# Kernel tuning notes

Measured on AMD Instinct MI355X. Metric: run time of the kernel, lower is better.

## Reference

```python
import jax, jax.numpy as jnp
import numpy as np

B, S, D, H = 2, 2048, 512, 8
HD = D // H
DFF = 4 * D
EPS_LN = 1e-5
EPS_ATTN = 1e-8


def layernorm(x, w, b):
    mu = jnp.mean(x, axis=-1, keepdims=True)
    var = jnp.var(x, axis=-1, keepdims=True)
    return (x - mu) * jax.lax.rsqrt(var + EPS_LN) * w + b


def masked_attention(q_src, v_src, wq, bq, wk, bk, wv, bv, wo, bo, M):
    # q_src/v_src: (B,S,D); M: (B,S,S)
    Bs, Ss, _ = q_src.shape
    Q = (q_src @ wq + bq).reshape(Bs, Ss, H, HD)
    K = (q_src @ wk + bk).reshape(Bs, Ss, H, HD)
    V = (v_src @ wv + bv).reshape(Bs, Ss, H, HD)
    scale = HD ** -0.5
    scores = jnp.einsum('bqhd,bkhd->bhqk', Q, K) * scale
    Mh = M[:, None, :, :]                      # (B,1,S,S) broadcast over heads
    scores = scores * Mh
    A = jax.nn.softmax(scores, axis=-1)
    A = A * Mh                                 # re-mask post-softmax
    A = A / (jnp.sum(jnp.abs(A), axis=-1, keepdims=True) + EPS_ATTN)  # L1 renorm
    out = jnp.einsum('bhqk,bkhd->bqhd', A, V).reshape(Bs, Ss, D)
    return out @ wo + bo


def ffn(x, w1, b1, w2, b2):
    h = jax.nn.gelu(x @ w1 + b1, approximate=False)
    return x + (h @ w2 + b2)                   # FeedForward(num_layers=2) includes residual


def setup_inputs() -> dict:
    key = jax.random.key(0)
    ks = iter(jax.random.split(key, 64))
    nrm = lambda shape, s=0.02: jax.random.normal(next(ks), shape, jnp.float32) * s
    d = {
        'gene_emb': jax.random.normal(next(ks), (B, S, D), jnp.float32),
        'expr_emb': jax.random.normal(next(ks), (B, S, D), jnp.float32),
        'M': jax.random.uniform(next(ks), (B, S, S), jnp.float32),
    }
    # gene attention params (weights stored (in,out))
    for p in ['g_wq', 'g_wk', 'g_wv', 'g_wo']:
        d[p] = nrm((D, D))
    for p in ['g_bq', 'g_bk', 'g_bv', 'g_bo']:
        d[p] = jnp.zeros((D,), jnp.float32)
    # expr attention params (fused proj 2D->D)
    d['e_wf'] = nrm((2 * D, D)); d['e_bf'] = jnp.zeros((D,), jnp.float32)
    for p in ['e_wq', 'e_wk', 'e_wv', 'e_wo']:
        d[p] = nrm((D, D))
    for p in ['e_bq', 'e_bk', 'e_bv', 'e_bo']:
        d[p] = jnp.zeros((D,), jnp.float32)
    # layernorms
    for p in ['ln_g1_w', 'ln_g2_w', 'ln_e1_w', 'ln_e2_w']:
        d[p] = jnp.ones((D,), jnp.float32)
    for p in ['ln_g1_b', 'ln_g2_b', 'ln_e1_b', 'ln_e2_b']:
        d[p] = jnp.zeros((D,), jnp.float32)
    # FFNs
    d['fg_w1'] = nrm((D, DFF)); d['fg_b1'] = jnp.zeros((DFF,), jnp.float32)
    d['fg_w2'] = nrm((DFF, D)); d['fg_b2'] = jnp.zeros((D,), jnp.float32)
    d['fe_w1'] = nrm((D, DFF)); d['fe_b1'] = jnp.zeros((DFF,), jnp.float32)
    d['fe_w2'] = nrm((DFF, D)); d['fe_b2'] = jnp.zeros((D,), jnp.float32)
    return d


def reference(gene_emb, expr_emb, M,
              g_wq, g_bq, g_wk, g_bk, g_wv, g_bv, g_wo, g_bo,
              e_wf, e_bf, e_wq, e_bq, e_wk, e_bk, e_wv, e_bv, e_wo, e_bo,
              ln_g1_w, ln_g1_b, ln_g2_w, ln_g2_b,
              ln_e1_w, ln_e1_b, ln_e2_w, ln_e2_b,
              fg_w1, fg_b1, fg_w2, fg_b2,
              fe_w1, fe_b1, fe_w2, fe_b2):
    # ----- gene branch -----
    xg = layernorm(gene_emb, ln_g1_w, ln_g1_b)
    attn_g = masked_attention(xg, xg, g_wq, g_bq, g_wk, g_bk, g_wv, g_bv, g_wo, g_bo, M)
    x = gene_emb + attn_g
    x_ln = layernorm(x, ln_g2_w, ln_g2_b)
    out_gene = x + ffn(x_ln, fg_w1, fg_b1, fg_w2, fg_b2)
    # ----- expression branch -----
    y_n = layernorm(expr_emb, ln_e1_w, ln_e1_b)
    fused = jnp.concatenate([gene_emb, y_n], axis=-1) @ e_wf + e_bf
    attn_e = masked_attention(fused, y_n, e_wq, e_bq, e_wk, e_bk, e_wv, e_bv, e_wo, e_bo, M)
    y = expr_emb + attn_e
    y_ln = layernorm(y, ln_e2_w, ln_e2_b)
    out_expr = y + ffn(y_ln, fe_w1, fe_b1, fe_w2, fe_b2)
    return (out_gene, out_expr)
```

## Files before the change

### kernel.cpp

```cpp
#include <hip/hip_runtime.h>
#include <math.h>

#define S_LEN 2048
#define DMODEL 512
#define NROWS 4096
#define NHEAD 8
#define HDIM 64
#define LOG2E 1.4426950408889634f

typedef __attribute__((ext_vector_type(8))) __bf16 bf16x8;
typedef __attribute__((ext_vector_type(4))) float f32x4;

__device__ inline float bf2f(unsigned short h) {
    unsigned u = ((unsigned)h) << 16;
    return __builtin_bit_cast(float, u);
}
__device__ inline unsigned short f2bf(float f) {
    unsigned u = __builtin_bit_cast(unsigned, f);
    return (unsigned short)((u + 0x7fffu + ((u >> 16) & 1u)) >> 16);
}

__device__ inline void gl_lds16(const unsigned short* g, unsigned short* l) {
    __builtin_amdgcn_global_load_lds(
        (const __attribute__((address_space(1))) void*)g,
        (__attribute__((address_space(3))) void*)l, 16, 0, 0);
}

__global__ __launch_bounds__(256) void wcast_t(
    const float* __restrict__ W, unsigned short* __restrict__ Wt, int K, int Mo)
{
    __shared__ float t[32][33];
    const int bx = blockIdx.x * 32;
    const int by = blockIdx.y * 32;
    const int tx = threadIdx.x & 31, ty = threadIdx.x >> 5;
    #pragma unroll
    for (int r = 0; r < 4; ++r)
        t[ty + 8 * r][tx] = W[(size_t)(by + ty + 8 * r) * Mo + bx + tx];
    __syncthreads();
    #pragma unroll
    for (int r = 0; r < 4; ++r)
        Wt[(size_t)(bx + ty + 8 * r) * K + by + tx] = f2bf(t[tx][ty + 8 * r]);
}

__global__ __launch_bounds__(256) void wcast_sq8(
    const float* w0, const float* w1, const float* w2, const float* w3,
    const float* w4, const float* w5, const float* w6, const float* w7,
    unsigned short* __restrict__ dst)
{
    const float* srcs[8] = {w0, w1, w2, w3, w4, w5, w6, w7};
    const float* __restrict__ W = srcs[blockIdx.z];
    unsigned short* __restrict__ Wt = dst + (size_t)blockIdx.z * 512 * 512;
    __shared__ float t[32][33];
    const int bx = blockIdx.x * 32, by = blockIdx.y * 32;
    const int tx = threadIdx.x & 31, ty = threadIdx.x >> 5;
    #pragma unroll
    for (int r = 0; r < 4; ++r)
        t[ty + 8 * r][tx] = W[(size_t)(by + ty + 8 * r) * 512 + bx + tx];
    __syncthreads();
    #pragma unroll
    for (int r = 0; r < 4; ++r)
        Wt[(size_t)(bx + ty + 8 * r) * 512 + by + tx] = f2bf(t[tx][ty + 8 * r]);
}

__global__ __launch_bounds__(256) void wcast_t2(
    const float* wA, const float* wB, unsigned short* __restrict__ dst,
    int K, int Mo)
{
    const float* __restrict__ W = blockIdx.z ? wB : wA;
    unsigned short* __restrict__ Wt = dst + (size_t)blockIdx.z * K * Mo;
    __shared__ float t[32][33];
    const int bx = blockIdx.x * 32, by = blockIdx.y * 32;
    const int tx = threadIdx.x & 31, ty = threadIdx.x >> 5;
    #pragma unroll
    for (int r = 0; r < 4; ++r)
        t[ty + 8 * r][tx] = W[(size_t)(by + ty + 8 * r) * Mo + bx + tx];
    __syncthreads();
    #pragma unroll
    for (int r = 0; r < 4; ++r)
        Wt[(size_t)(bx + ty + 8 * r) * K + by + tx] = f2bf(t[tx][ty + 8 * r]);
}

__global__ __launch_bounds__(256) void pack_bias(
    const float* __restrict__ b1, const float* __restrict__ b2,
    const float* __restrict__ b3, float* __restrict__ dst, int n)
{
    int t = blockIdx.x * 256 + threadIdx.x;
    if (t >= n) return;
    float v = (t < 512) ? b1[t] : (t < 1024) ? b2[t - 512] : b3[t - 1024];
    dst[t] = v;
}

__global__ __launch_bounds__(256) void cast_strided(
    const float* __restrict__ in, unsigned short* __restrict__ out, int ostride)
{
    const int row = blockIdx.x, t = threadIdx.x;
    out[(size_t)row * ostride + t]       = f2bf(in[(size_t)row * DMODEL + t]);
    out[(size_t)row * ostride + t + 256] = f2bf(in[(size_t)row * DMODEL + t + 256]);
}

__global__ __launch_bounds__(256) void ln_kernel(
    const float* __restrict__ x, const float* __restrict__ w,
    const float* __restrict__ b, unsigned short* __restrict__ y, int ostride)
{
    __shared__ float red[8];
    const int row = blockIdx.x;
    const float* xr = x + (size_t)row * DMODEL;
    const int t = threadIdx.x;
    float v0 = xr[t];
    float v1 = xr[t + 256];
    float s  = v0 + v1;
    float sq = v0 * v0 + v1 * v1;
    #pragma unroll
    for (int o = 32; o > 0; o >>= 1) {
        s  += __shfl_down(s, o);
        sq += __shfl_down(sq, o);
    }
    int wid = t >> 6, lane = t & 63;
    if (lane == 0) { red[wid] = s; red[4 + wid] = sq; }
    __syncthreads();
    float mean = (red[0] + red[1] + red[2] + red[3]) * (1.0f / 512.0f);
    float msq  = (red[4] + red[5] + red[6] + red[7]) * (1.0f / 512.0f);
    float var  = msq - mean * mean;
    float rs   = rsqrtf(var + 1e-5f);
    y[(size_t)row * ostride + t]       = f2bf((v0 - mean) * rs * w[t] + b[t]);
    y[(size_t)row * ostride + t + 256] = f2bf((v1 - mean) * rs * w[t + 256] + b[t + 256]);
}

__global__ __launch_bounds__(256) void vtrans(
    const unsigned short* __restrict__ V, int ldv, unsigned short* __restrict__ Vt)
{
    __shared__ unsigned short t[64][72];
    const int s0 = blockIdx.x * 64, h = blockIdx.y, b = blockIdx.z;
    const int tid = threadIdx.x;
    {
        const int r = tid >> 2, c = (tid & 3) * 16;
        const unsigned short* src = V + (size_t)(b * S_LEN + s0 + r) * ldv + h * 64 + c;
        *(int4*)&t[r][c]     = *(const int4*)(src);
        *(int4*)&t[r][c + 8] = *(const int4*)(src + 8);
    }
    __syncthreads();
    {
        const int d = tid >> 2, s = (tid & 3) * 16;
        unsigned short* dst = Vt + ((size_t)((b * 8 + h) * 64 + d)) * S_LEN + s0 + s;
        unsigned short tmp[16];
        #pragma unroll
        for (int e = 0; e < 16; ++e) tmp[e] = t[s + e][d];
        *(int4*)dst       = *(int4*)&tmp[0];
        *(int4*)(dst + 8) = *(int4*)&tmp[8];
    }
}

__global__ __launch_bounds__(256) void gemm_mfma(
    const unsigned short* __restrict__ A, int lda,
    const unsigned short* __restrict__ Bt,
    const float* __restrict__ bias,
    const float* __restrict__ R1,
    const unsigned short* __restrict__ R2,
    float* __restrict__ Cf, unsigned short* __restrict__ Cb,
    int K, int Mo, int dogelu)
{
    __shared__ __align__(16) unsigned short As[128 * 32];
    __shared__ __align__(16) unsigned short Bs[128 * 32];
    const int tid = threadIdx.x;
    const int wave = tid >> 6, lane = tid & 63;
    const int wr = wave >> 1, wc = wave & 1;
    const int row0 = blockIdx.y * 128, col0 = blockIdx.x * 128;
    const int l15 = lane & 15, q = lane >> 4;

    f32x4 acc[4][4];
    const f32x4 zz = {0.f, 0.f, 0.f, 0.f};
    #pragma unroll
    for (int i = 0; i < 4; ++i)
        #pragma unroll
        for (int j = 0; j < 4; ++j) acc[i][j] = zz;

    for (int k0 = 0; k0 < K; k0 += 32) {
        #pragma unroll
        for (int r = 0; r < 2; ++r) {
            int idx = r * 256 + tid;
            int row = idx >> 2, kc = idx & 3;
            gl_lds16(&A[(size_t)(row0 + row) * lda + k0 + kc * 8],
                     &As[(size_t)(r * 256 + wave * 64) * 8]);
            gl_lds16(&Bt[(size_t)(col0 + row) * K + k0 + kc * 8],
                     &Bs[(size_t)(r * 256 + wave * 64) * 8]);
        }
        __syncthreads();
        bf16x8 af[4], bfr[4];
        #pragma unroll
        for (int fi = 0; fi < 4; ++fi)
            af[fi] = *(const bf16x8*)&As[(wr * 64 + fi * 16 + l15) * 32 + q * 8];
        #pragma unroll
        for (int fj = 0; fj < 4; ++fj)
            bfr[fj] = *(const bf16x8*)&Bs[(wc * 64 + fj * 16 + l15) * 32 + q * 8];
        #pragma unroll
        for (int fi = 0; fi < 4; ++fi)
            #pragma unroll
            for (int fj = 0; fj < 4; ++fj)
                acc[fi][fj] = __builtin_amdgcn_mfma_f32_16x16x32_bf16(
                    af[fi], bfr[fj], acc[fi][fj], 0, 0, 0);
        __syncthreads();
    }

    #pragma unroll
    for (int fi = 0; fi < 4; ++fi) {
        #pragma unroll
        for (int reg = 0; reg < 4; ++reg) {
            int row = row0 + wr * 64 + fi * 16 + q * 4 + reg;
            #pragma unroll
            for (int fj = 0; fj < 4; ++fj) {
                int col = col0 + wc * 64 + fj * 16 + l15;
                float v = acc[fi][fj][reg] + bias[col];
                if (dogelu) v = 0.5f * v * (1.0f + erff(v * 0.70710678118654752f));
                size_t off = (size_t)row * Mo + col;
                if (R1) v += R1[off];
                if (R2) v += bf2f(R2[off]);
                if (Cb) Cb[off] = f2bf(v);
                else    Cf[off] = v;
            }
        }
    }
}

__global__ __launch_bounds__(256) void gemm_mfma64(
    const unsigned short* __restrict__ A, int lda,
    const unsigned short* __restrict__ Bt,
    const float* __restrict__ bias,
    const float* __restrict__ R1,
    const unsigned short* __restrict__ R2,
    float* __restrict__ Cf, unsigned short* __restrict__ Cb,
    int K, int Mo, int dogelu)
{
    __shared__ __align__(16) unsigned short As[64 * 64];
    __shared__ __align__(16) unsigned short Bs[64 * 64];
    const int tid = threadIdx.x;
    const int wave = tid >> 6, lane = tid & 63;
    const int row0 = blockIdx.y * 64, col0 = blockIdx.x * 64;
    const int l15 = lane & 15, q = lane >> 4;

    f32x4 acc[4];
    const f32x4 zz = {0.f, 0.f, 0.f, 0.f};
    #pragma unroll
    for (int j = 0; j < 4; ++j) acc[j] = zz;

    for (int k0 = 0; k0 < K; k0 += 64) {
        #pragma unroll
        for (int r = 0; r < 2; ++r) {
            int idx = r * 256 + tid;
            int row = idx >> 3, kc = idx & 7;
            gl_lds16(&A[(size_t)(row0 + row) * lda + k0 + kc * 8],
                     &As[(size_t)(r * 256 + wave * 64) * 8]);
            gl_lds16(&Bt[(size_t)(col0 + row) * K + k0 + kc * 8],
                     &Bs[(size_t)(r * 256 + wave * 64) * 8]);
        }
        __syncthreads();
        #pragma unroll
        for (int ks = 0; ks < 2; ++ks) {
            bf16x8 af = *(const bf16x8*)&As[(wave * 16 + l15) * 64 + ks * 32 + q * 8];
            bf16x8 bfr[4];
            #pragma unroll
            for (int fj = 0; fj < 4; ++fj)
                bfr[fj] = *(const bf16x8*)&Bs[(fj * 16 + l15) * 64 + ks * 32 + q * 8];
            #pragma unroll
            for (int fj = 0; fj < 4; ++fj)
                acc[fj] = __builtin_amdgcn_mfma_f32_16x16x32_bf16(af, bfr[fj], acc[fj], 0, 0, 0);
        }
        __syncthreads();
    }

    #pragma unroll
    for (int reg = 0; reg < 4; ++reg) {
        int row = row0 + wave * 16 + q * 4 + reg;
        #pragma unroll
        for (int fj = 0; fj < 4; ++fj) {
            int col = col0 + fj * 16 + l15;
            float v = acc[fj][reg] + bias[col];
            if (dogelu) v = 0.5f * v * (1.0f + erff(v * 0.70710678118654752f));
            size_t off = (size_t)row * Mo + col;
            if (R1) v += R1[off];
            if (R2) v += bf2f(R2[off]);
            if (Cb) Cb[off] = f2bf(v);
            else    Cf[off] = v;
        }
    }
}

__global__ __launch_bounds__(256, 4) void attn_mfma_split(
    const unsigned short* __restrict__ Q, int ldq,
    const unsigned short* __restrict__ Kp, int ldk,
    const unsigned short* __restrict__ Vt,
    const float* __restrict__ M,
    unsigned short* __restrict__ Opart,
    float* __restrict__ stats)
{
    __shared__ __align__(16) unsigned short Ks[64 * 72];
    __shared__ __align__(16) unsigned short Vs[64 * 72];
    __shared__ __align__(16) unsigned short Ps_all[4][16 * 72];

    const int bh = blockIdx.y, b = bh >> 3, h = bh & 7;
    const int q0 = blockIdx.x * 64;
    const int p = blockIdx.z;
    const int tid = threadIdx.x, wave = tid >> 6, lane = tid & 63;
    const int l15 = lane & 15, quad = lane >> 4;
    const int iRow = q0 + wave * 16 + l15;
    const int kBeg = p * (S_LEN / 2), kEnd = kBeg + (S_LEN / 2);

    unsigned short* Ps = &Ps_all[wave][0];

    bf16x8 qf[2];
    {
        const unsigned short* qp = Q + (size_t)(b * S_LEN + iRow) * ldq + h * HDIM + quad * 8;
        #pragma unroll
        for (int ks = 0; ks < 2; ++ks) {
            union { bf16x8 v; unsigned short u[8]; } tq;
            tq.v = *(const bf16x8*)(qp + ks * 32);
            #pragma unroll
            for (int e = 0; e < 8; ++e)
                tq.u[e] = f2bf(bf2f(tq.u[e]) * (0.125f * LOG2E));
            qf[ks] = tq.v;
        }
    }

    const int srow = tid >> 3;
    const int scol = (tid & 7) * 8;
    const unsigned short* kg = Kp + ((size_t)b * S_LEN) * ldk + h * HDIM + scol;
    const unsigned short* vg = Vt + ((size_t)bh * 64 + srow) * S_LEN + scol;
    const float* mrow = M + ((size_t)b * S_LEN + iRow) * S_LEN + quad * 4;

    float rm = -INFINITY, rZ = 0.f, rZm = 0.f;
    f32x4 oacc[4];
    const f32x4 zz = {0.f, 0.f, 0.f, 0.f};
    #pragma unroll
    for (int dt = 0; dt < 4; ++dt) oacc[dt] = zz;

    int4 kv0 = *(const int4*)(kg + (size_t)(kBeg + srow) * ldk);
    int4 kv1 = *(const int4*)(kg + (size_t)(kBeg + srow + 32) * ldk);
    int4 vv0 = *(const int4*)(vg + kBeg);
    int4 vv1 = *(const int4*)(vg + 32 * S_LEN + kBeg);
    *(int4*)&Ks[srow * 72 + scol]        = kv0;
    *(int4*)&Ks[(srow + 32) * 72 + scol] = kv1;
    *(int4*)&Vs[srow * 72 + scol]        = vv0;
    *(int4*)&Vs[(srow + 32) * 72 + scol] = vv1;
    __syncthreads();

    for (int k0 = kBeg; k0 < kEnd; k0 += 64) {
        const bool more = (k0 + 64 < kEnd);
        if (more) {
            kv0 = *(const int4*)(kg + (size_t)(k0 + 64 + srow) * ldk);
            kv1 = *(const int4*)(kg + (size_t)(k0 + 64 + srow + 32) * ldk);
            vv0 = *(const int4*)(vg + k0 + 64);
            vv1 = *(const int4*)(vg + 32 * S_LEN + k0 + 64);
        }
        float4 m4[4];
        #pragma unroll
        for (int jt = 0; jt < 4; ++jt)
            m4[jt] = *(const float4*)(mrow + k0 + jt * 16);

        f32x4 sacc[4];
        #pragma unroll
        for (int jt = 0; jt < 4; ++jt) sacc[jt] = zz;
        __builtin_amdgcn_s_setprio(1);
        #pragma unroll
        for (int jt = 0; jt < 4; ++jt) {
            bf16x8 kf0 = *(const bf16x8*)&Ks[(jt * 16 + l15) * 72 + quad * 8];
            bf16x8 kf1 = *(const bf16x8*)&Ks[(jt * 16 + l15) * 72 + 32 + quad * 8];
            sacc[jt] = __builtin_amdgcn_mfma_f32_16x16x32_bf16(kf0, qf[0], sacc[jt], 0, 0, 0);
            sacc[jt] = __builtin_amdgcn_mfma_f32_16x16x32_bf16(kf1, qf[1], sacc[jt], 0, 0, 0);
        }
        __builtin_amdgcn_s_setprio(0);

        float mx = -INFINITY;
        #pragma unroll
        for (int jt = 0; jt < 4; ++jt) {
            float mm[4] = {m4[jt].x, m4[jt].y, m4[jt].z, m4[jt].w};
            #pragma unroll
            for (int r = 0; r < 4; ++r) {
                sacc[jt][r] = sacc[jt][r] * mm[r];
                mx = fmaxf(mx, sacc[jt][r]);
            }
        }
        mx = fmaxf(mx, __shfl_xor(mx, 16));
        mx = fmaxf(mx, __shfl_xor(mx, 32));
        if (!__all(mx <= rm + 8.0f)) {
            float mn = fmaxf(rm, mx);
            float al = __builtin_amdgcn_exp2f(rm - mn);
            rm = mn; rZ *= al; rZm *= al;
            #pragma unroll
            for (int dt = 0; dt < 4; ++dt)
                #pragma unroll
                for (int r = 0; r < 4; ++r) oacc[dt][r] *= al;
        }

        float z = 0.f, zm = 0.f;
        #pragma unroll
        for (int jt = 0; jt < 4; ++jt) {
            float mm[4] = {m4[jt].x, m4[jt].y, m4[jt].z, m4[jt].w};
            float pv[4];
            #pragma unroll
            for (int r = 0; r < 4; ++r) {
                float e = __builtin_amdgcn_exp2f(sacc[jt][r] - rm);
                float pm = e * mm[r];
                z += e; zm += pm; pv[r] = pm;
            }
            unsigned lo, hi;
            asm("v_cvt_pk_bf16_f32 %0, %1, %2" : "=v"(lo) : "v"(pv[0]), "v"(pv[1]));
            asm("v_cvt_pk_bf16_f32 %0, %1, %2" : "=v"(hi) : "v"(pv[2]), "v"(pv[3]));
            uint2 pk; pk.x = lo; pk.y = hi;
            *(uint2*)&Ps[l15 * 72 + jt * 16 + quad * 4] = pk;
        }
        z  += __shfl_xor(z, 16);  z  += __shfl_xor(z, 32);
        zm += __shfl_xor(zm, 16); zm += __shfl_xor(zm, 32);
        rZ += z; rZm += zm;

        bf16x8 pf0 = *(const bf16x8*)&Ps[l15 * 72 + quad * 8];
        bf16x8 pf1 = *(const bf16x8*)&Ps[l15 * 72 + 32 + quad * 8];
        __builtin_amdgcn_s_setprio(1);
        #pragma unroll
        for (int dt = 0; dt < 4; ++dt) {
            bf16x8 vf0 = *(const bf16x8*)&Vs[(dt * 16 + l15) * 72 + quad * 8];
            bf16x8 vf1 = *(const bf16x8*)&Vs[(dt * 16 + l15) * 72 + 32 + quad * 8];
            oacc[dt] = __builtin_amdgcn_mfma_f32_16x16x32_bf16(vf0, pf0, oacc[dt], 0, 0, 0);
            oacc[dt] = __builtin_amdgcn_mfma_f32_16x16x32_bf16(vf1, pf1, oacc[dt], 0, 0, 0);
        }
        __builtin_amdgcn_s_setprio(0);

        if (more) {
            __syncthreads();
            *(int4*)&Ks[srow * 72 + scol]        = kv0;
            *(int4*)&Ks[(srow + 32) * 72 + scol] = kv1;
            *(int4*)&Vs[srow * 72 + scol]        = vv0;
            *(int4*)&Vs[(srow + 32) * 72 + scol] = vv1;
            __syncthreads();
        }
    }

    unsigned short* op = Opart + (((size_t)(p * 16 + bh) * S_LEN + iRow) * 64);
    #pragma unroll
    for (int dt = 0; dt < 4; ++dt) {
        unsigned lo, hi;
        asm("v_cvt_pk_bf16_f32 %0, %1, %2" : "=v"(lo) : "v"(oacc[dt][0]), "v"(oacc[dt][1]));
        asm("v_cvt_pk_bf16_f32 %0, %1, %2" : "=v"(hi) : "v"(oacc[dt][2]), "v"(oacc[dt][3]));
        uint2 o2; o2.x = lo; o2.y = hi;
        *(uint2*)(op + dt * 16 + quad * 4) = o2;
    }
    if (quad == 0) {
        float4 st; st.x = rm; st.y = rZ; st.z = rZm; st.w = 0.f;
        *(float4*)&stats[(((size_t)p * 16 + bh) * S_LEN + iRow) * 4] = st;
    }
}

__global__ __launch_bounds__(256) void attn_combine(
    const unsigned short* __restrict__ Opart, const float* __restrict__ stats,
    unsigned short* __restrict__ O)
{
    const int bh = blockIdx.y, b = bh >> 3, h = bh & 7;
    const int q0 = blockIdx.x * 64;
    const int tid = threadIdx.x;
    const int i = tid >> 2, dq = (tid & 3) * 16;
    const int qg = q0 + i;

    float4 s0 = *(const float4*)&stats[(((size_t)0 * 16 + bh) * S_LEN + qg) * 4];
    float4 s1 = *(const float4*)&stats[(((size_t)1 * 16 + bh) * S_LEN + qg) * 4];
    float ms = fmaxf(s0.x, s1.x);
    float w0 = __builtin_amdgcn_exp2f(s0.x - ms), w1 = __builtin_amdgcn_exp2f(s1.x - ms);
    float Z  = w0 * s0.y + w1 * s1.y;
    float Zm = w0 * s0.z + w1 * s1.z;
    float inv = 1.0f / (Zm + 1e-8f * Z);
    w0 *= inv; w1 *= inv;

    const unsigned short* p0 = Opart + (((size_t)0 * 16 + bh) * S_LEN + qg) * 64 + dq;
    const unsigned short* p1 = Opart + (((size_t)1 * 16 + bh) * S_LEN + qg) * 64 + dq;
    union { int4 v; unsigned short u[8]; } a0, a1, r;
    unsigned short* dst = O + (size_t)(b * S_LEN + qg) * DMODEL + h * HDIM + dq;
    #pragma unroll
    for (int half = 0; half < 2; ++half) {
        a0.v = *(const int4*)(p0 + half * 8);
        a1.v = *(const int4*)(p1 + half * 8);
        #pragma unroll
        for (int e = 0; e < 8; ++e)
            r.u[e] = f2bf(w0 * bf2f(a0.u[e]) + w1 * bf2f(a1.u[e]));
        *(int4*)(dst + half * 8) = r.v;
    }
}

extern "C" void kernel_launch(void* const* d_in, const int* in_sizes, int n_in,
                              void* d_out, int out_size, void* d_ws, size_t ws_size,
                              hipStream_t stream)
{
    const float* gene_emb = (const float*)d_in[0];
    const float* expr_emb = (const float*)d_in[1];
    const float* M        = (const float*)d_in[2];
    const float* g_wq = (const float*)d_in[3];
    const float* g_wk = (const float*)d_in[4];
    const float* g_wv = (const float*)d_in[5];
    const float* g_wo = (const float*)d_in[6];
    const float* g_bq = (const float*)d_in[7];
    const float* g_bk = (const float*)d_in[8];
    const float* g_bv = (const float*)d_in[9];
    const float* g_bo = (const float*)d_in[10];
    const float* e_wf = (const float*)d_in[11];
    const float* e_bf = (const float*)d_in[12];
    const float* e_wq = (const float*)d_in[13];
    const float* e_wk = (const float*)d_in[14];
    const float* e_wv = (const float*)d_in[15];
    const float* e_wo = (const float*)d_in[16];
    const float* e_bq = (const float*)d_in[17];
    const float* e_bk = (const float*)d_in[18];
    const float* e_bv = (const float*)d_in[19];
    const float* e_bo = (const float*)d_in[20];
    const float* ln_g1_w = (const float*)d_in[21];
    const float* ln_g2_w = (const float*)d_in[22];
    const float* ln_e1_w = (const float*)d_in[23];
    const float* ln_e2_w = (const float*)d_in[24];
    const float* ln_g1_b = (const float*)d_in[25];
    const float* ln_g2_b = (const float*)d_in[26];
    const float* ln_e1_b = (const float*)d_in[27];
    const float* ln_e2_b = (const float*)d_in[28];
    const float* fg_w1 = (const float*)d_in[29];
    const float* fg_b1 = (const float*)d_in[30];
    const float* fg_w2 = (const float*)d_in[31];
    const float* fg_b2 = (const float*)d_in[32];
    const float* fe_w1 = (const float*)d_in[33];
    const float* fe_b1 = (const float*)d_in[34];
    const float* fe_w2 = (const float*)d_in[35];
    const float* fe_b2 = (const float*)d_in[36];

    float* out_gene = (float*)d_out;
    float* out_expr = out_gene + (size_t)NROWS * DMODEL;

    char* ws = (char*)d_ws;
    const size_t MB1 = 1024 * 1024;
    unsigned short* bufA16  = (unsigned short*)(ws + 0 * MB1);
    unsigned short* bufAt16 = (unsigned short*)(ws + 4 * MB1);
    unsigned short* bufQKV  = (unsigned short*)(ws + 8 * MB1);
    unsigned short* bufQKe  = (unsigned short*)(ws + 8 * MB1);
    unsigned short* bufV16  = (unsigned short*)(ws + 16 * MB1);
    unsigned short* bufVt   = (unsigned short*)(ws + 20 * MB1);
    unsigned short* bufCat  = (unsigned short*)(ws + 24 * MB1);
    unsigned short* bufOp   = (unsigned short*)(ws + 24 * MB1);
    float*          bufSt   = (float*)(ws + 32 * MB1);
    float*          bufX    = (float*)(ws + 33 * MB1);
    unsigned short* bufH16  = (unsigned short*)(ws + 8 * MB1);
    char* wp = ws + 41 * MB1;
    unsigned short* sq8    = (unsigned short*)wp;
    unsigned short* gwq_t  = sq8 + 0 * 512 * 512;
    unsigned short* gwk_t  = sq8 + 1 * 512 * 512;
    unsigned short* gwv_t  = sq8 + 2 * 512 * 512;
    unsigned short* gwo_t  = sq8 + 3 * 512 * 512;
    unsigned short* ewq_t  = sq8 + 4 * 512 * 512;
    unsigned short* ewk_t  = sq8 + 5 * 512 * 512;
    unsigned short* ewv_t  = sq8 + 6 * 512 * 512;
    unsigned short* ewo_t  = sq8 + 7 * 512 * 512;
    unsigned short* ewf_t  = sq8 + 8 * 512 * 512;
    unsigned short* ffn1   = ewf_t + 1024 * 512;
    unsigned short* fgw1_t = ffn1;
    unsigned short* few1_t = ffn1 + 512 * 2048;
    unsigned short* ffn2   = few1_t + 512 * 2048;
    unsigned short* fgw2_t = ffn2;
    unsigned short* few2_t = ffn2 + 2048 * 512;
    float* biasg = (float*)(few2_t + 2048 * 512);
    float* biase = biasg + 1536;

    dim3 blk(256);
    dim3 ln_grid(NROWS);
    dim3 g512s(8, 64);
    dim3 g1024(8, 32);
    dim3 g1536(12, 32);
    dim3 g2048(16, 32);
    dim3 attn_grid(S_LEN / 64, 16, 2);
    dim3 comb_grid(S_LEN / 64, 16);
    dim3 vt_grid(S_LEN / 64, NHEAD, 2);

    wcast_sq8<<<dim3(16, 16, 8), blk, 0, stream>>>(
        g_wq, g_wk, g_wv, g_wo, e_wq, e_wk, e_wv, e_wo, sq8);
    wcast_t<<<dim3(16, 32), blk, 0, stream>>>(e_wf, ewf_t, 1024, 512);
    wcast_t2<<<dim3(64, 16, 2), blk, 0, stream>>>(fg_w1, fe_w1, ffn1, 512, 2048);
    wcast_t2<<<dim3(16, 64, 2), blk, 0, stream>>>(fg_w2, fe_w2, ffn2, 2048, 512);
    pack_bias<<<dim3(6), blk, 0, stream>>>(g_bq, g_bk, g_bv, biasg, 1536);
    pack_bias<<<dim3(4), blk, 0, stream>>>(e_bq, e_bk, e_bk, biase, 1024);

    ln_kernel<<<ln_grid, blk, 0, stream>>>(gene_emb, ln_g1_w, ln_g1_b, bufA16, 512);
    gemm_mfma<<<g1536, blk, 0, stream>>>(bufA16, 512, gwq_t, biasg, nullptr, nullptr, nullptr, bufQKV, 512, 1536, 0);
    vtrans<<<vt_grid, blk, 0, stream>>>(bufQKV + 1024, 1536, bufVt);
    attn_mfma_split<<<attn_grid, blk, 0, stream>>>(bufQKV, 1536, bufQKV + 512, 1536, bufVt, M, bufOp, bufSt);
    attn_combine<<<comb_grid, blk, 0, stream>>>(bufOp, bufSt, bufAt16);
    gemm_mfma64<<<g512s, blk, 0, stream>>>(bufAt16, 512, gwo_t, g_bo, gene_emb, nullptr, bufX, nullptr, 512, 512, 0);
    ln_kernel<<<ln_grid, blk, 0, stream>>>(bufX, ln_g2_w, ln_g2_b, bufA16, 512);
    gemm_mfma<<<g2048, blk, 0, stream>>>(bufA16, 512, fgw1_t, fg_b1, nullptr, nullptr, nullptr, bufH16, 512, 2048, 1);
    gemm_mfma64<<<g512s, blk, 0, stream>>>(bufH16, 2048, fgw2_t, fg_b2, bufX, bufA16, out_gene, nullptr, 2048, 512, 0);

    cast_strided<<<ln_grid, blk, 0, stream>>>(gene_emb, bufCat, 1024);
    ln_kernel<<<ln_grid, blk, 0, stream>>>(expr_emb, ln_e1_w, ln_e1_b, bufCat + 512, 1024);
    gemm_mfma64<<<g512s, blk, 0, stream>>>(bufCat, 1024, ewf_t, e_bf, nullptr, nullptr, nullptr, bufA16, 1024, 512, 0);
    gemm_mfma<<<g1024, blk, 0, stream>>>(bufA16, 512, ewq_t, biase, nullptr, nullptr, nullptr, bufQKe, 512, 1024, 0);
    gemm_mfma64<<<g512s, blk, 0, stream>>>(bufCat + 512, 1024, ewv_t, e_bv, nullptr, nullptr, nullptr, bufV16, 512, 512, 0);
    vtrans<<<vt_grid, blk, 0, stream>>>(bufV16, 512, bufVt);
    attn_mfma_split<<<attn_grid, blk, 0, stream>>>(bufQKe, 1024, bufQKe + 512, 1024, bufVt, M, bufOp, bufSt);
    attn_combine<<<comb_grid, blk, 0, stream>>>(bufOp, bufSt, bufAt16);
    gemm_mfma64<<<g512s, blk, 0, stream>>>(bufAt16, 512, ewo_t, e_bo, expr_emb, nullptr, bufX, nullptr, 512, 512, 0);
    ln_kernel<<<ln_grid, blk, 0, stream>>>(bufX, ln_e2_w, ln_e2_b, bufA16, 512);
    gemm_mfma<<<g2048, blk, 0, stream>>>(bufA16, 512, few1_t, fe_b1, nullptr, nullptr, nullptr, bufH16, 512, 2048, 1);
    gemm_mfma64<<<g512s, blk, 0, stream>>>(bufH16, 2048, few2_t, fe_b2, bufX, bufA16, out_expr, nullptr, 2048, 512, 0);
}
```

Before: 539.1 us.

## Double-buffer LDS tiles in both MFMA GEMMs and swizzle the 64-wide tile

Both bf16 MFMA GEMM kernels now keep two LDS buffers per operand. Each iteration issues the async global-to-LDS loads for the next K slice before running the MFMAs on the current slice, so memory latency overlaps with compute. The 64x64 kernel also XOR-swizzles the 16-byte chunk positions within each LDS row to cut bank conflicts on the fragment reads. The cost is twice the LDS per block, which may lower occupancy, and the overlap relies on the barrier's wait for the async loads.

Measured after the change: 522.1 us. -3.1%, faster.

```diff
diff --git a/kernel.cpp b/kernel.cpp
--- a/kernel.cpp
+++ b/kernel.cpp
@@ -159,8 +159,8 @@
     float* __restrict__ Cf, unsigned short* __restrict__ Cb,
     int K, int Mo, int dogelu)
 {
-    __shared__ __align__(16) unsigned short As[128 * 32];
-    __shared__ __align__(16) unsigned short Bs[128 * 32];
+    __shared__ __align__(16) unsigned short As[2][128 * 32];
+    __shared__ __align__(16) unsigned short Bs[2][128 * 32];
     const int tid = threadIdx.x;
     const int wave = tid >> 6, lane = tid & 63;
     const int wr = wave >> 1, wc = wave & 1;
@@ -174,24 +174,39 @@
         #pragma unroll
         for (int j = 0; j < 4; ++j) acc[i][j] = zz;
 
-    for (int k0 = 0; k0 < K; k0 += 32) {
-        #pragma unroll
-        for (int r = 0; r < 2; ++r) {
-            int idx = r * 256 + tid;
-            int row = idx >> 2, kc = idx & 3;
-            gl_lds16(&A[(size_t)(row0 + row) * lda + k0 + kc * 8],
-                     &As[(size_t)(r * 256 + wave * 64) * 8]);
-            gl_lds16(&Bt[(size_t)(col0 + row) * K + k0 + kc * 8],
-                     &Bs[(size_t)(r * 256 + wave * 64) * 8]);
-        }
-        __syncthreads();
+    const int nk = K >> 5;
+    #pragma unroll
+    for (int r = 0; r < 2; ++r) {
+        int idx = r * 256 + tid;
+        int row = idx >> 2, kc = idx & 3;
+        gl_lds16(&A[(size_t)(row0 + row) * lda + kc * 8],
+                 &As[0][(size_t)(r * 256 + wave * 64) * 8]);
+        gl_lds16(&Bt[(size_t)(col0 + row) * K + kc * 8],
+                 &Bs[0][(size_t)(r * 256 + wave * 64) * 8]);
+    }
+    __syncthreads();
+
+    for (int t = 0; t < nk; ++t) {
+        const int cur = t & 1;
+        if (t + 1 < nk) {
+            const int k0 = (t + 1) * 32;
+            #pragma unroll
+            for (int r = 0; r < 2; ++r) {
+                int idx = r * 256 + tid;
+                int row = idx >> 2, kc = idx & 3;
+                gl_lds16(&A[(size_t)(row0 + row) * lda + k0 + kc * 8],
+                         &As[cur ^ 1][(size_t)(r * 256 + wave * 64) * 8]);
+                gl_lds16(&Bt[(size_t)(col0 + row) * K + k0 + kc * 8],
+                         &Bs[cur ^ 1][(size_t)(r * 256 + wave * 64) * 8]);
+            }
+        }
         bf16x8 af[4], bfr[4];
         #pragma unroll
         for (int fi = 0; fi < 4; ++fi)
-            af[fi] = *(const bf16x8*)&As[(wr * 64 + fi * 16 + l15) * 32 + q * 8];
+            af[fi] = *(const bf16x8*)&As[cur][(wr * 64 + fi * 16 + l15) * 32 + q * 8];
         #pragma unroll
         for (int fj = 0; fj < 4; ++fj)
-            bfr[fj] = *(const bf16x8*)&Bs[(wc * 64 + fj * 16 + l15) * 32 + q * 8];
+            bfr[fj] = *(const bf16x8*)&Bs[cur][(wc * 64 + fj * 16 + l15) * 32 + q * 8];
         #pragma unroll
         for (int fi = 0; fi < 4; ++fi)
             #pragma unroll
@@ -230,8 +245,8 @@
     float* __restrict__ Cf, unsigned short* __restrict__ Cb,
     int K, int Mo, int dogelu)
 {
-    __shared__ __align__(16) unsigned short As[64 * 64];
-    __shared__ __align__(16) unsigned short Bs[64 * 64];
+    __shared__ __align__(16) unsigned short As[2][64 * 64];
+    __shared__ __align__(16) unsigned short Bs[2][64 * 64];
     const int tid = threadIdx.x;
     const int wave = tid >> 6, lane = tid & 63;
     const int row0 = blockIdx.y * 64, col0 = blockIdx.x * 64;
@@ -242,24 +257,42 @@
     #pragma unroll
     for (int j = 0; j < 4; ++j) acc[j] = zz;
 
-    for (int k0 = 0; k0 < K; k0 += 64) {
-        #pragma unroll
-        for (int r = 0; r < 2; ++r) {
-            int idx = r * 256 + tid;
-            int row = idx >> 3, kc = idx & 7;
-            gl_lds16(&A[(size_t)(row0 + row) * lda + k0 + kc * 8],
-                     &As[(size_t)(r * 256 + wave * 64) * 8]);
-            gl_lds16(&Bt[(size_t)(col0 + row) * K + k0 + kc * 8],
-                     &Bs[(size_t)(r * 256 + wave * 64) * 8]);
-        }
-        __syncthreads();
+    const int nk = K >> 6;
+    #pragma unroll
+    for (int r = 0; r < 2; ++r) {
+        int idx = r * 256 + tid;
+        int row = idx >> 3;
+        int kc  = (idx & 7) ^ (row & 7);
+        gl_lds16(&A[(size_t)(row0 + row) * lda + kc * 8],
+                 &As[0][(size_t)(r * 256 + wave * 64) * 8]);
+        gl_lds16(&Bt[(size_t)(col0 + row) * K + kc * 8],
+                 &Bs[0][(size_t)(r * 256 + wave * 64) * 8]);
+    }
+    __syncthreads();
+
+    for (int t = 0; t < nk; ++t) {
+        const int cur = t & 1;
+        if (t + 1 < nk) {
+            const int k0 = (t + 1) * 64;
+            #pragma unroll
+            for (int r = 0; r < 2; ++r) {
+                int idx = r * 256 + tid;
+                int row = idx >> 3;
+                int kc  = (idx & 7) ^ (row & 7);
+                gl_lds16(&A[(size_t)(row0 + row) * lda + k0 + kc * 8],
+                         &As[cur ^ 1][(size_t)(r * 256 + wave * 64) * 8]);
+                gl_lds16(&Bt[(size_t)(col0 + row) * K + k0 + kc * 8],
+                         &Bs[cur ^ 1][(size_t)(r * 256 + wave * 64) * 8]);
+            }
+        }
         #pragma unroll
         for (int ks = 0; ks < 2; ++ks) {
-            bf16x8 af = *(const bf16x8*)&As[(wave * 16 + l15) * 64 + ks * 32 + q * 8];
+            const int cx = ((ks * 4 + q) ^ (l15 & 7)) * 8;
+            bf16x8 af = *(const bf16x8*)&As[cur][(wave * 16 + l15) * 64 + cx];
             bf16x8 bfr[4];
             #pragma unroll
             for (int fj = 0; fj < 4; ++fj)
-                bfr[fj] = *(const bf16x8*)&Bs[(fj * 16 + l15) * 64 + ks * 32 + q * 8];
+                bfr[fj] = *(const bf16x8*)&Bs[cur][(fj * 16 + l15) * 64 + cx];
             #pragma unroll
             for (int fj = 0; fj < 4; ++fj)
                 acc[fj] = __builtin_amdgcn_mfma_f32_16x16x32_bf16(af, bfr[fj], acc[fj], 0, 0, 0);
```
